# Kernel optimization log

Measured on AMD Instinct MI355X. Metric: run time of the kernel, lower is better.

The kernel has to match this reference:

```python
import jax, jax.numpy as jnp
import numpy as np

B, J, C = 8, 2048, 256
K = 32
H = 8
D = 32  # out_dim per head


def setup_inputs() -> dict:
    key = jax.random.key(0)
    k0, k1, k2, k3, k4, k5 = jax.random.split(key, 6)
    x = jax.random.normal(k0, (B, J, C), dtype=jnp.float32)
    nbr_idx = jax.random.randint(k1, (B, J, K), 0, J)
    s_in = 1.0 / np.sqrt(C)
    s_hd = 1.0 / np.sqrt(H * D)
    Wq = jax.random.uniform(k2, (C, H * D), dtype=jnp.float32, minval=-s_in, maxval=s_in)
    Wk = jax.random.uniform(k3, (C, H * D), dtype=jnp.float32, minval=-s_in, maxval=s_in)
    Wv = jax.random.uniform(k4, (C, H * D), dtype=jnp.float32, minval=-s_in, maxval=s_in)
    Wp = jax.random.uniform(k5, (H * D, D), dtype=jnp.float32, minval=-s_hd, maxval=s_hd)
    return {"x": x, "nbr_idx": nbr_idx, "Wq": Wq, "Wk": Wk, "Wv": Wv, "Wp": Wp}


def reference(x, nbr_idx, Wq, Wk, Wv, Wp):
    b, j, c = x.shape
    q = (x @ Wq).reshape(b, j, H, D)  # [B,J,H,D]
    k = (x @ Wk).reshape(b, j, H, D)
    v = (x @ Wv).reshape(b, j, H, D)
    bidx = jnp.arange(b)[:, None, None]  # [B,1,1]
    k_nbr = k[bidx, nbr_idx]  # [B,J,K,H,D]
    v_nbr = v[bidx, nbr_idx]  # [B,J,K,H,D]
    attn = jnp.einsum("bjhd,bjkhd->bjkh", q, k_nbr) / np.sqrt(D)
    attn = jax.nn.leaky_relu(attn, negative_slope=0.2)
    attn = jax.nn.softmax(attn, axis=2)  # softmax over K neighbors
    out = jnp.einsum("bjkh,bjkhd->bjhd", attn, v_nbr).reshape(b, j, H * D)
    return out @ Wp  # [B,J,D]
```

## Files before the change

### kernel.cpp

```cpp
#include <hip/hip_runtime.h>
#include <hip/hip_bf16.h>


typedef short bf16x8 __attribute__((ext_vector_type(8)));
typedef float f32x4  __attribute__((ext_vector_type(4)));
typedef float f32x2  __attribute__((ext_vector_type(2)));

__device__ __forceinline__ float bf2f(unsigned short u) {
    union { unsigned int i; float f; } c; c.i = ((unsigned int)u) << 16; return c.f;
}
__device__ __forceinline__ unsigned short f2bf(float f) {
    union { float f; unsigned int i; } c; c.f = f;
    unsigned int r = c.i + 0x7FFFu + ((c.i >> 16) & 1u);
    return (unsigned short)(r >> 16);
}
__device__ __forceinline__ f32x2 upk(unsigned int u) {
    union { unsigned int i; float f; } lo, hi;
    lo.i = u << 16;
    hi.i = u & 0xffff0000u;
    return (f32x2){lo.f, hi.f};
}

__device__ __forceinline__ void gld_lds16(void* lds, const void* g) {
    __builtin_amdgcn_global_load_lds(
        (const __attribute__((address_space(1))) unsigned int*)g,
        (__attribute__((address_space(3))) unsigned int*)lds,
        16, 0, 0);
}

__global__ __launch_bounds__(256) void prep(
    const float* __restrict__ x,
    const float* __restrict__ Wq, const float* __restrict__ Wk,
    const float* __restrict__ Wv, const float* __restrict__ Wp,
    unsigned short* __restrict__ xb, unsigned short* __restrict__ Wt)
{
    const int blk = blockIdx.x, tid = threadIdx.x;
    if (blk < 4096) {
        int t = blk * 256 + tid;
        float4 f = ((const float4*)x)[t];
        ushort4 u;
        u.x = f2bf(f.x); u.y = f2bf(f.y); u.z = f2bf(f.z); u.w = f2bf(f.w);
        ((ushort4*)xb)[t] = u;
        return;
    }
    int wi = blk - 4096;
    int w = wi >> 8, n = wi & 255, t = tid;
    if (w == 0) {
        Wt[(size_t)n * 256 + t] = f2bf(Wq[(size_t)t * 256 + n]);
    } else if (w == 1) {
        Wt[(size_t)(256 + n) * 256 + t] = f2bf(Wk[(size_t)t * 256 + n]);
    } else {
        int h = n >> 5, c = n & 31;
        float acc = 0.f;
#pragma unroll
        for (int d = 0; d < 32; d++)
            acc += Wv[(size_t)t * 256 + h * 32 + d] * Wp[(size_t)(h * 32 + d) * 32 + c];
        Wt[(size_t)(512 + n) * 256 + t] = f2bf(acc);
    }
}

__global__ __launch_bounds__(256) void qkv_mfma(
    const unsigned short* __restrict__ xb,
    const unsigned short* __restrict__ Wt,
    unsigned short* __restrict__ Q, unsigned short* __restrict__ Kp,
    unsigned short* __restrict__ VP)
{
    __shared__ unsigned short Als[128][64];
    __shared__ unsigned short Bls[128][64];

    const unsigned short* Wb = Wt + (size_t)blockIdx.z * 65536;
    unsigned short* Y = (blockIdx.z == 0) ? Q : (blockIdx.z == 1) ? Kp : VP;

    const int row0 = blockIdx.x * 128;
    const int col0 = blockIdx.y * 128;
    const int tid  = threadIdx.x;
    const int w    = tid >> 6, l = tid & 63;
    const int wm   = (w >> 1) * 64, wn = (w & 1) * 64;
    const int lm   = l & 15, quad = l >> 4;

    f32x4 acc[4][4];
#pragma unroll
    for (int i = 0; i < 4; i++)
#pragma unroll
        for (int j = 0; j < 4; j++) acc[i][j] = (f32x4){0.f, 0.f, 0.f, 0.f};

    const char* Ab = (const char*)(xb + (size_t)row0 * 256);
    const char* Bb = (const char*)(Wb + (size_t)col0 * 256);

    for (int k0 = 0; k0 < 256; k0 += 64) {
#pragma unroll
        for (int i = 0; i < 4; i++) {
            int s = i * 256 + tid;
            int r = s >> 3, c = s & 7;
            size_t go = (size_t)r * 512 + (size_t)k0 * 2 + c * 16;
            gld_lds16((char*)Als + s * 16, Ab + go);
            gld_lds16((char*)Bls + s * 16, Bb + go);
        }
        __syncthreads();

#pragma unroll
        for (int kk = 0; kk < 64; kk += 32) {
            bf16x8 a[4], b[4];
#pragma unroll
            for (int tm = 0; tm < 4; tm++)
                a[tm] = *(const bf16x8*)&Als[wm + tm * 16 + lm][kk + quad * 8];
#pragma unroll
            for (int tn = 0; tn < 4; tn++)
                b[tn] = *(const bf16x8*)&Bls[wn + tn * 16 + lm][kk + quad * 8];
#pragma unroll
            for (int tm = 0; tm < 4; tm++)
#pragma unroll
                for (int tn = 0; tn < 4; tn++)
                    acc[tm][tn] = __builtin_amdgcn_mfma_f32_16x16x32_bf16(
                        a[tm], b[tn], acc[tm][tn], 0, 0, 0);
        }
        __syncthreads();
    }

#pragma unroll
    for (int tm = 0; tm < 4; tm++) {
        int rbase = row0 + wm + tm * 16 + quad * 4;
#pragma unroll
        for (int tn = 0; tn < 4; tn++) {
            int col = col0 + wn + tn * 16 + lm;
#pragma unroll
            for (int r = 0; r < 4; r++)
                Y[(size_t)(rbase + r) * 256 + col] = f2bf(acc[tm][tn][r]);
        }
    }
}

__global__ __launch_bounds__(256) void attn_all(
    const unsigned short* __restrict__ qb,
    const unsigned short* __restrict__ kb,
    const unsigned short* __restrict__ vp,
    const int*            __restrict__ nbr,
    float*                __restrict__ out)
{
    __shared__ int   koff[32];
    __shared__ float sc[8 * 33];
    __shared__ float pw[8 * 33];
    __shared__ float redB[8 * 264];
    __shared__ float red2[256];

    const int b   = blockIdx.x & 7;
    const int j   = blockIdx.x >> 3;
    const int bj  = (b << 11) + j;
    const int tid = threadIdx.x;

    if (tid < 32) koff[tid] = nbr[(size_t)bj * 32 + tid] << 8;

    const int w    = tid >> 6;
    const int l    = tid & 63;
    const int lh   = l & 31;
    const int half = l >> 5;
    const int hA   = lh >> 2;
    const int g    = 2 * w + half;
    const size_t bbase = (size_t)b << 19;

    uint4 qu = *(const uint4*)(qb + (size_t)bj * 256 + lh * 8);
    __syncthreads();

    uint4 ku[4], vu[4];
#pragma unroll
    for (int p = 0; p < 4; p++) {
        const int kkA = w * 8 + 2 * p + half;
        ku[p] = *(const uint4*)(kb + bbase + koff[kkA] + lh * 8);
    }
#pragma unroll
    for (int p = 0; p < 4; p++) {
        const int kkB = p * 8 + g;
        vu[p] = *(const uint4*)(vp + bbase + koff[kkB] + lh * 8);
    }

    f32x2 qf[4];
    qf[0] = upk(qu.x); qf[1] = upk(qu.y); qf[2] = upk(qu.z); qf[3] = upk(qu.w);

#pragma unroll
    for (int p = 0; p < 4; p++) {
        const int kkA = w * 8 + 2 * p + half;
        f32x2 a2 = (f32x2){0.f, 0.f};
        a2 += upk(ku[p].x) * qf[0];
        a2 += upk(ku[p].y) * qf[1];
        a2 += upk(ku[p].z) * qf[2];
        a2 += upk(ku[p].w) * qf[3];
        float acc = a2.x + a2.y;
        acc += __shfl_xor(acc, 1);
        acc += __shfl_xor(acc, 2);
        if ((l & 3) == 0) {
            float s = acc * 0.17677669529663687f;
            s = (s > 0.f) ? s : 0.2f * s;
            sc[hA * 33 + kkA] = s;
        }
    }
    __syncthreads();

    {
        const int h2  = 2 * w + half;
        const int kk2 = lh;
        float s = sc[h2 * 33 + kk2];
        float mx = s;
#pragma unroll
        for (int m = 16; m >= 1; m >>= 1) mx = fmaxf(mx, __shfl_xor(mx, m));
        float e = __expf(s - mx);
        float sum = e;
#pragma unroll
        for (int m = 16; m >= 1; m >>= 1) sum += __shfl_xor(sum, m);
        pw[h2 * 33 + kk2] = e / sum;
    }
    __syncthreads();

    {
        f32x2 a0 = (f32x2){0.f,0.f}, a1 = a0, a2v = a0, a3 = a0;
#pragma unroll
        for (int p = 0; p < 4; p++) {
            const int kkB = p * 8 + g;
            const float wgt = pw[hA * 33 + kkB];
            const f32x2 w2 = (f32x2){wgt, wgt};
            a0  += upk(vu[p].x) * w2;
            a1  += upk(vu[p].y) * w2;
            a2v += upk(vu[p].z) * w2;
            a3  += upk(vu[p].w) * w2;
        }
        float* rb = &redB[g * 264 + lh * 8];
        *(float4*)(rb)     = make_float4(a0.x, a0.y, a1.x, a1.y);
        *(float4*)(rb + 4) = make_float4(a2v.x, a2v.y, a3.x, a3.y);
    }
    __syncthreads();

    {
        float s = 0.f;
#pragma unroll
        for (int gg = 0; gg < 8; gg++) s += redB[gg * 264 + tid];
        red2[tid] = s;
    }
    __syncthreads();

    if (tid < 32) {
        float o = 0.f;
#pragma unroll
        for (int h = 0; h < 8; h++) o += red2[h * 32 + tid];
        out[(size_t)bj * 32 + tid] = o;
    }
}

__global__ __launch_bounds__(256) void fused_all(
    const float* __restrict__ X, const int* __restrict__ nbr,
    const float* __restrict__ Wq, const float* __restrict__ Wk,
    const float* __restrict__ Wv, const float* __restrict__ Wp,
    float* __restrict__ out)
{
    __shared__ float xr[256], qrow[256], xn[256];
    __shared__ float vn[32][256];
    __shared__ int   nb[32];
    __shared__ float sc[32][8], pwv[32][8];
    __shared__ float sp[256], hd[256];
    __shared__ float red[8][32];

    const int bj = blockIdx.x, b = bj >> 11, tid = threadIdx.x;

    xr[tid] = X[(size_t)bj * 256 + tid];
    if (tid < 32) nb[tid] = nbr[(size_t)bj * 32 + tid];
    __syncthreads();

    {
        float acc = 0.f;
#pragma unroll 8
        for (int c = 0; c < 256; c++) acc += xr[c] * Wq[(size_t)c * 256 + tid];
        qrow[tid] = acc;
    }
    __syncthreads();

    for (int i = 0; i < 32; i++) {
        size_t r = (size_t)(b * 2048 + nb[i]);
        xn[tid] = X[r * 256 + tid];
        __syncthreads();
        float ka = 0.f, va = 0.f;
#pragma unroll 8
        for (int c = 0; c < 256; c++) {
            float xc = xn[c];
            ka += xc * Wk[(size_t)c * 256 + tid];
            va += xc * Wv[(size_t)c * 256 + tid];
        }
        vn[i][tid] = va;
        sp[tid] = qrow[tid] * ka;
        __syncthreads();
        if (tid < 8) {
            float s = 0.f;
#pragma unroll
            for (int d = 0; d < 32; d++) s += sp[tid * 32 + d];
            s *= 0.17677669529663687f;
            s = (s > 0.f) ? s : 0.2f * s;
            sc[i][tid] = s;
        }
        __syncthreads();
    }

    {
        const int h = tid & 7, kk = tid >> 3;
        float mx = -1e30f;
#pragma unroll
        for (int i = 0; i < 32; i++) mx = fmaxf(mx, sc[i][h]);
        float ssum = 0.f;
#pragma unroll
        for (int i = 0; i < 32; i++) ssum += __expf(sc[i][h] - mx);
        pwv[kk][h] = __expf(sc[kk][h] - mx) / ssum;
    }
    __syncthreads();

    {
        const int h2 = tid >> 5;
        float acc = 0.f;
#pragma unroll 8
        for (int i = 0; i < 32; i++) acc += pwv[i][h2] * vn[i][tid];
        hd[tid] = acc;
    }
    __syncthreads();

    {
        const int c = tid & 31, ch = tid >> 5;
        float p = 0.f;
#pragma unroll
        for (int i = 0; i < 32; i++) { int r = ch * 32 + i; p += hd[r] * Wp[r * 32 + c]; }
        red[ch][c] = p;
    }
    __syncthreads();

    if (tid < 32) {
        float o = 0.f;
#pragma unroll
        for (int i = 0; i < 8; i++) o += red[i][tid];
        out[(size_t)bj * 32 + tid] = o;
    }
}

extern "C" void kernel_launch(void* const* d_in, const int* in_sizes, int n_in,
                              void* d_out, int out_size, void* d_ws, size_t ws_size,
                              hipStream_t stream) {
    const float* x   = (const float*)d_in[0];
    const int*   nbr = (const int*)d_in[1];
    const float* Wq  = (const float*)d_in[2];
    const float* Wk  = (const float*)d_in[3];
    const float* Wv  = (const float*)d_in[4];
    const float* Wp  = (const float*)d_in[5];
    float*       out = (float*)d_out;

    const size_t ME   = (size_t)16384 * 256;
    const size_t need = (4 * ME + 3 * 65536) * sizeof(unsigned short);

    if (ws_size >= need) {
        unsigned short* q  = (unsigned short*)d_ws;
        unsigned short* k  = q + ME;
        unsigned short* vp = k + ME;
        unsigned short* xb = vp + ME;
        unsigned short* Wt = xb + ME;

        prep<<<4096 + 768, 256, 0, stream>>>(x, Wq, Wk, Wv, Wp, xb, Wt);
        qkv_mfma<<<dim3(128, 2, 3), 256, 0, stream>>>(xb, Wt, q, k, vp);
        attn_all<<<16384, 256, 0, stream>>>(q, k, vp, nbr, out);
    } else {
        fused_all<<<16384, 256, 0, stream>>>(x, nbr, Wq, Wk, Wv, Wp, out);
    }
}
```

Baseline: 124.9 us.

## Process two query rows per block in the neighbor attention kernel

Each attn_all block now handles two consecutive query rows instead of one, and the grid is halved. The neighbor indices for both rows are staged together, and the score and softmax stages run for both rows inside one set of barriers. The aim is to spread per-block launch, index-load and barrier overhead over more work. In exchange, the V gathers are no longer issued before the score phase but only after the softmax barrier, so their latency is less hidden. The output reduction is also serialized per row, adding extra barriers.

```diff
diff --git a/kernel.cpp b/kernel.cpp
--- a/kernel.cpp
+++ b/kernel.cpp
@@ -137,18 +137,18 @@
     const int*            __restrict__ nbr,
     float*                __restrict__ out)
 {
-    __shared__ int   koff[32];
-    __shared__ float sc[8 * 33];
-    __shared__ float pw[8 * 33];
+    __shared__ int   koff[64];
+    __shared__ float sc[2][8 * 33];
+    __shared__ float pw[2][8 * 33];
     __shared__ float redB[8 * 264];
     __shared__ float red2[256];
 
     const int b   = blockIdx.x & 7;
-    const int j   = blockIdx.x >> 3;
-    const int bj  = (b << 11) + j;
+    const int jt  = blockIdx.x >> 3;
+    const int bj0 = (b << 11) + jt * 2;
     const int tid = threadIdx.x;
 
-    if (tid < 32) koff[tid] = nbr[(size_t)bj * 32 + tid] << 8;
+    if (tid < 64) koff[tid] = nbr[(size_t)bj0 * 32 + tid] << 8;
 
     const int w    = tid >> 6;
     const int l    = tid & 63;
@@ -158,39 +158,32 @@
     const int g    = 2 * w + half;
     const size_t bbase = (size_t)b << 19;
 
-    uint4 qu = *(const uint4*)(qb + (size_t)bj * 256 + lh * 8);
-    __syncthreads();
-
-    uint4 ku[4], vu[4];
-#pragma unroll
-    for (int p = 0; p < 4; p++) {
-        const int kkA = w * 8 + 2 * p + half;
-        ku[p] = *(const uint4*)(kb + bbase + koff[kkA] + lh * 8);
-    }
-#pragma unroll
-    for (int p = 0; p < 4; p++) {
-        const int kkB = p * 8 + g;
-        vu[p] = *(const uint4*)(vp + bbase + koff[kkB] + lh * 8);
-    }
-
-    f32x2 qf[4];
-    qf[0] = upk(qu.x); qf[1] = upk(qu.y); qf[2] = upk(qu.z); qf[3] = upk(qu.w);
-
-#pragma unroll
-    for (int p = 0; p < 4; p++) {
-        const int kkA = w * 8 + 2 * p + half;
-        f32x2 a2 = (f32x2){0.f, 0.f};
-        a2 += upk(ku[p].x) * qf[0];
-        a2 += upk(ku[p].y) * qf[1];
-        a2 += upk(ku[p].z) * qf[2];
-        a2 += upk(ku[p].w) * qf[3];
-        float acc = a2.x + a2.y;
-        acc += __shfl_xor(acc, 1);
-        acc += __shfl_xor(acc, 2);
-        if ((l & 3) == 0) {
-            float s = acc * 0.17677669529663687f;
-            s = (s > 0.f) ? s : 0.2f * s;
-            sc[hA * 33 + kkA] = s;
+    uint4 qu0 = *(const uint4*)(qb + (size_t)(bj0 + 0) * 256 + lh * 8);
+    uint4 qu1 = *(const uint4*)(qb + (size_t)(bj0 + 1) * 256 + lh * 8);
+    __syncthreads();
+
+#pragma unroll
+    for (int ql = 0; ql < 2; ql++) {
+        uint4 qu = ql ? qu1 : qu0;
+        f32x2 qf[4];
+        qf[0] = upk(qu.x); qf[1] = upk(qu.y); qf[2] = upk(qu.z); qf[3] = upk(qu.w);
+#pragma unroll
+        for (int p = 0; p < 4; p++) {
+            const int kkA = w * 8 + 2 * p + half;
+            uint4 u = *(const uint4*)(kb + bbase + koff[ql * 32 + kkA] + lh * 8);
+            f32x2 a2 = (f32x2){0.f, 0.f};
+            a2 += upk(u.x) * qf[0];
+            a2 += upk(u.y) * qf[1];
+            a2 += upk(u.z) * qf[2];
+            a2 += upk(u.w) * qf[3];
+            float acc = a2.x + a2.y;
+            acc += __shfl_xor(acc, 1);
+            acc += __shfl_xor(acc, 2);
+            if ((l & 3) == 0) {
+                float s = acc * 0.17677669529663687f;
+                s = (s > 0.f) ? s : 0.2f * s;
+                sc[ql][hA * 33 + kkA] = s;
+            }
         }
     }
     __syncthreads();
@@ -198,29 +191,44 @@
     {
         const int h2  = 2 * w + half;
         const int kk2 = lh;
-        float s = sc[h2 * 33 + kk2];
-        float mx = s;
-#pragma unroll
-        for (int m = 16; m >= 1; m >>= 1) mx = fmaxf(mx, __shfl_xor(mx, m));
-        float e = __expf(s - mx);
-        float sum = e;
-#pragma unroll
-        for (int m = 16; m >= 1; m >>= 1) sum += __shfl_xor(sum, m);
-        pw[h2 * 33 + kk2] = e / sum;
-    }
-    __syncthreads();
-
+#pragma unroll
+        for (int ql = 0; ql < 2; ql++) {
+            float s = sc[ql][h2 * 33 + kk2];
+            float mx = s;
+#pragma unroll
+            for (int m = 16; m >= 1; m >>= 1) mx = fmaxf(mx, __shfl_xor(mx, m));
+            float e = __expf(s - mx);
+            float sum = e;
+#pragma unroll
+            for (int m = 16; m >= 1; m >>= 1) sum += __shfl_xor(sum, m);
+            pw[ql][h2 * 33 + kk2] = e / sum;
+        }
+    }
+    __syncthreads();
+
+    uint4 vu1[4];
     {
         f32x2 a0 = (f32x2){0.f,0.f}, a1 = a0, a2v = a0, a3 = a0;
+        uint4 vu0[4];
 #pragma unroll
         for (int p = 0; p < 4; p++) {
             const int kkB = p * 8 + g;
-            const float wgt = pw[hA * 33 + kkB];
+            vu0[p] = *(const uint4*)(vp + bbase + koff[kkB] + lh * 8);
+        }
+#pragma unroll
+        for (int p = 0; p < 4; p++) {
+            const int kkB = p * 8 + g;
+            vu1[p] = *(const uint4*)(vp + bbase + koff[32 + kkB] + lh * 8);
+        }
+#pragma unroll
+        for (int p = 0; p < 4; p++) {
+            const int kkB = p * 8 + g;
+            const float wgt = pw[0][hA * 33 + kkB];
             const f32x2 w2 = (f32x2){wgt, wgt};
-            a0  += upk(vu[p].x) * w2;
-            a1  += upk(vu[p].y) * w2;
-            a2v += upk(vu[p].z) * w2;
-            a3  += upk(vu[p].w) * w2;
+            a0  += upk(vu0[p].x) * w2;
+            a1  += upk(vu0[p].y) * w2;
+            a2v += upk(vu0[p].z) * w2;
+            a3  += upk(vu0[p].w) * w2;
         }
         float* rb = &redB[g * 264 + lh * 8];
         *(float4*)(rb)     = make_float4(a0.x, a0.y, a1.x, a1.y);
@@ -240,7 +248,39 @@
         float o = 0.f;
 #pragma unroll
         for (int h = 0; h < 8; h++) o += red2[h * 32 + tid];
-        out[(size_t)bj * 32 + tid] = o;
+        out[(size_t)(bj0 + 0) * 32 + tid] = o;
+    }
+    {
+        f32x2 a0 = (f32x2){0.f,0.f}, a1 = a0, a2v = a0, a3 = a0;
+#pragma unroll
+        for (int p = 0; p < 4; p++) {
+            const int kkB = p * 8 + g;
+            const float wgt = pw[1][hA * 33 + kkB];
+            const f32x2 w2 = (f32x2){wgt, wgt};
+            a0  += upk(vu1[p].x) * w2;
+            a1  += upk(vu1[p].y) * w2;
+            a2v += upk(vu1[p].z) * w2;
+            a3  += upk(vu1[p].w) * w2;
+        }
+        float* rb = &redB[g * 264 + lh * 8];
+        *(float4*)(rb)     = make_float4(a0.x, a0.y, a1.x, a1.y);
+        *(float4*)(rb + 4) = make_float4(a2v.x, a2v.y, a3.x, a3.y);
+    }
+    __syncthreads();
+
+    {
+        float s = 0.f;
+#pragma unroll
+        for (int gg = 0; gg < 8; gg++) s += redB[gg * 264 + tid];
+        red2[tid] = s;
+    }
+    __syncthreads();
+
+    if (tid < 32) {
+        float o = 0.f;
+#pragma unroll
+        for (int h = 0; h < 8; h++) o += red2[h * 32 + tid];
+        out[(size_t)(bj0 + 1) * 32 + tid] = o;
     }
 }
 
@@ -357,7 +397,7 @@
 
         prep<<<4096 + 768, 256, 0, stream>>>(x, Wq, Wk, Wv, Wp, xb, Wt);
         qkv_mfma<<<dim3(128, 2, 3), 256, 0, stream>>>(xb, Wt, q, k, vp);
-        attn_all<<<16384, 256, 0, stream>>>(q, k, vp, nbr, out);
+        attn_all<<<8192, 256, 0, stream>>>(q, k, vp, nbr, out);
     } else {
         fused_all<<<16384, 256, 0, stream>>>(x, nbr, Wq, Wk, Wv, Wp, out);
     }
```

Measured after the change: 126.2 us. About the same (+1.0%).
